# Performance work log

Measured on AMD Instinct MI355X. Metric: run time of the kernel, lower is better.

## Reference

```python
import jax, jax.numpy as jnp
import numpy as np

V, H, L, B = 32000, 512, 128, 8
PAD = 0


def setup_inputs() -> dict:
    key = jax.random.key(0)
    ks = jax.random.split(key, 20)
    s = 0.02
    inp = {
        "input_": jax.random.randint(ks[0], (B, L), 0, V),
        "encoder_inputs": jax.random.randint(ks[1], (B, L), 0, V),
        "encoder_hidden": jax.random.normal(ks[2], (1, B, H), jnp.float32),
        "encoder_outputs": jax.random.normal(ks[3], (B, L, H), jnp.float32),
        "emb_table": jax.random.normal(ks[4], (V, H), jnp.float32) * s,
        "attn_W": jax.random.normal(ks[5], (L, 2 * H), jnp.float32) * s,
        "attn_b": jnp.zeros((L,), jnp.float32),
        "comb_W": jax.random.normal(ks[6], (H, 2 * H), jnp.float32) * s,
        "comb_b": jnp.zeros((H,), jnp.float32),
        "gru_Wih": jax.random.normal(ks[7], (3 * H, H), jnp.float32) * s,
        "gru_Whh": jax.random.normal(ks[8], (3 * H, H), jnp.float32) * s,
        "gru_bih": jnp.zeros((3 * H,), jnp.float32),
        "gru_bhh": jnp.zeros((3 * H,), jnp.float32),
        "out_W": jax.random.normal(ks[9], (V, H), jnp.float32) * s,
        "out_b": jnp.zeros((V,), jnp.float32),
        "dogen_W": jax.random.normal(ks[10], (1, 3 * H), jnp.float32) * s,
        "dogen_b": jnp.zeros((1,), jnp.float32),
        "copy_W": jax.random.normal(ks[11], (1, 2 * H), jnp.float32) * s,
        "copy_b": jnp.zeros((1,), jnp.float32),
    }
    return inp


def _gru(x, h0, Wih, Whh, bih, bhh):
    # x: [B,L,H] batch_first; h0: [B,H]. PyTorch GRU gate math.
    def step(h, x_t):
        gi = x_t @ Wih.T + bih  # [B,3H]
        gh = h @ Whh.T + bhh
        i_r, i_z, i_n = jnp.split(gi, 3, axis=-1)
        h_r, h_z, h_n = jnp.split(gh, 3, axis=-1)
        r = jax.nn.sigmoid(i_r + h_r)
        z = jax.nn.sigmoid(i_z + h_z)
        n = jnp.tanh(i_n + r * h_n)
        h_new = (1.0 - z) * n + z * h
        return h_new, h_new
    _, ys = jax.lax.scan(step, h0, jnp.swapaxes(x, 0, 1))  # ys: [L,B,H]
    return jnp.swapaxes(ys, 0, 1)


def reference(input_, encoder_inputs, encoder_hidden, encoder_outputs, emb_table,
              attn_W, attn_b, comb_W, comb_b, gru_Wih, gru_Whh, gru_bih, gru_bhh,
              out_W, out_b, dogen_W, dogen_b, copy_W, copy_b):
    # Dropout is identity (eval mode).
    embedded = emb_table[input_]  # [B,L,H]
    h0 = encoder_hidden[0]  # [B,H]
    hid_exp = jnp.broadcast_to(h0[:, None, :], embedded.shape)
    attn_logits = jnp.concatenate([embedded, hid_exp], axis=2) @ attn_W.T + attn_b  # [B,L,L]
    attn_weights = jax.nn.softmax(attn_logits, axis=1)  # softmax over dim=1 (as in torch code)
    attn_applied = jnp.einsum('bij,bjh->bih', attn_weights, encoder_outputs)
    x = jnp.concatenate([embedded, attn_applied], axis=2) @ comb_W.T + comb_b
    x = jax.nn.relu(x)
    output = _gru(x, h0, gru_Wih, gru_Whh, gru_bih, gru_bhh)  # [B,L,H]
    generation_dist = jax.nn.softmax(output @ out_W.T + out_b, axis=2)  # [B,L,V]
    # get_alpha: copy_weight_proj is rank-1 over concat([e_states, d_states]);
    # compute without materializing the [B,L,L,2H] cross product.
    w_e, w_d = copy_W[0, :H], copy_W[0, H:]
    e_part = encoder_outputs @ w_e  # [B,L] (indexed by j)
    d_part = output @ w_d           # [B,L] (indexed by i)
    logits = d_part[:, :, None] + e_part[:, None, :] + copy_b[0]  # [B,L_dec,L_enc]
    pad_pen = jnp.where(encoder_inputs == PAD, -1000.0, 0.0)
    logits = logits + pad_pen[:, None, :]
    alphas = jax.nn.softmax(logits, axis=2)
    context = jnp.einsum('bij,bjh->bih', alphas, encoder_outputs)
    # scatter_add: index repeats encoder_inputs[b,i] along j, so all alpha mass
    # of row (b,i) lands at vocab id encoder_inputs[b,i].
    row_sum = alphas.sum(axis=2)  # [B,L]
    b_idx = jnp.arange(B)[:, None]
    i_idx = jnp.arange(L)[None, :]
    copy_dist = jnp.zeros((B, L, V), generation_dist.dtype).at[b_idx, i_idx, encoder_inputs].add(row_sum)
    mix = jax.nn.sigmoid(jnp.concatenate([output, context, embedded], axis=2) @ dogen_W.T + dogen_b)  # [B,L,1]
    prob = generation_dist * mix + copy_dist * (1.0 - mix)
    return prob, attn_weights
```

## Files before the change

kernel.cpp:

```cpp
#include <hip/hip_runtime.h>
#include <cstdint>

#define VDIM 32000
#define HDIM 512
#define LDIM 128
#define BDIM 8
#define MROWS 1024
#define H2 1024
#define H3 1536
#define GRU_WGS 32

typedef __bf16 bf16x8 __attribute__((ext_vector_type(8)));
typedef float f32x4 __attribute__((ext_vector_type(4)));

#define AS1 __attribute__((address_space(1)))
#define AS3 __attribute__((address_space(3)))

__device__ __forceinline__ unsigned short f2b(float x) {
  unsigned u = __builtin_bit_cast(unsigned, x);
  u += 0x7fffu + ((u >> 16) & 1u);
  return (unsigned short)(u >> 16);
}

__device__ __forceinline__ float wredS(float v) {
#pragma unroll
  for (int o = 32; o > 0; o >>= 1) v += __shfl_xor(v, o);
  return v;
}
__device__ __forceinline__ float wredM(float v) {
#pragma unroll
  for (int o = 32; o > 0; o >>= 1) v = fmaxf(v, __shfl_xor(v, o));
  return v;
}

__device__ __forceinline__ void gl_lds16(const void* g, void* l) {
  __builtin_amdgcn_global_load_lds((AS1 void*)const_cast<void*>(g), (AS3 void*)l, 16, 0, 0);
}

__global__ void cvt_kernel(const float* __restrict__ src, unsigned short* __restrict__ dst, int n4) {
  int i = blockIdx.x * 256 + threadIdx.x;
  if (i < n4) {
    float4 v = ((const float4*)src)[i];
    unsigned r0 = (unsigned)f2b(v.x) | ((unsigned)f2b(v.y) << 16);
    unsigned r1 = (unsigned)f2b(v.z) | ((unsigned)f2b(v.w) << 16);
    uint2 r; r.x = r0; r.y = r1;
    *(uint2*)(dst + (size_t)i * 4) = r;
  }
}

__global__ void init_kernel(const float* __restrict__ h0, float* __restrict__ hbuf,
                            unsigned short* __restrict__ hbufbf, float* __restrict__ rowsum,
                            int* __restrict__ cnt) {
  int tid = threadIdx.x;
  for (int i = tid; i < BDIM * HDIM; i += 256) {
    float v = h0[i];
    hbuf[i] = v;
    hbufbf[i] = f2b(v);
  }
  for (int i = tid; i < MROWS; i += 256) rowsum[i] = 0.f;
  for (int i = tid; i < 160; i += 256) cnt[i] = (i == 0) ? GRU_WGS : 0;
}

__global__ void embed_kernel(const int* __restrict__ input_, const float* __restrict__ emb,
                             float* __restrict__ emb_f, unsigned short* __restrict__ A4) {
  int m = blockIdx.x, tid = threadIdx.x;
  int tok = input_[m];
  const float* src = emb + (size_t)tok * HDIM;
  for (int k = tid; k < HDIM; k += 256) {
    float v = src[k];
    emb_f[(size_t)m * HDIM + k] = v;
    A4[(size_t)m * H2 + k] = f2b(v);
  }
}

__global__ void attn_kernel(const float* __restrict__ emb_f, const float* __restrict__ h0,
                            const float* __restrict__ attn_W, const float* __restrict__ attn_b,
                            float* __restrict__ attn_out) {
  int j = blockIdx.x, b = blockIdx.y, tid = threadIdx.x;
  int wid = tid >> 6;
  __shared__ float wj[H2];
  __shared__ float red[2];
  for (int k = tid; k < H2; k += 128) wj[k] = attn_W[(size_t)j * H2 + k];
  __syncthreads();
  float hp = 0.f;
  for (int k = tid * 4; k < tid * 4 + 4; ++k) hp += h0[b * HDIM + k] * wj[HDIM + k];
  hp = wredS(hp);
  if ((tid & 63) == 0) red[wid] = hp;
  __syncthreads();
  float hdot = red[0] + red[1];
  __syncthreads();

  int i = tid;
  const float* er = emb_f + ((size_t)(b * LDIM + i)) * HDIM;
  float acc = 0.f;
  for (int k = 0; k < HDIM; k += 4) {
    float4 e = *(const float4*)(er + k);
    acc += e.x * wj[k] + e.y * wj[k + 1] + e.z * wj[k + 2] + e.w * wj[k + 3];
  }
  float l = acc + hdot + attn_b[j];
  float mx = wredM(l);
  if ((tid & 63) == 0) red[wid] = mx;
  __syncthreads();
  mx = fmaxf(red[0], red[1]);
  __syncthreads();
  float e = __expf(l - mx);
  float s = wredS(e);
  if ((tid & 63) == 0) red[wid] = s;
  __syncthreads();
  s = red[0] + red[1];
  attn_out[(size_t)b * (LDIM * LDIM) + (size_t)i * LDIM + j] = e / s;
}

__global__ void einsum_kernel(const float* __restrict__ w, const float* __restrict__ enc,
                              float* __restrict__ outF, unsigned short* __restrict__ outBf, int mode) {
  int i = blockIdx.x, b = blockIdx.y, tid = threadIdx.x;
  __shared__ float wr[LDIM];
  if (tid < LDIM) wr[tid] = w[((size_t)(b * LDIM + i)) * LDIM + tid];
  __syncthreads();
  float a0 = 0.f, a1 = 0.f;
  const float* eb = enc + (size_t)b * LDIM * HDIM;
  for (int jj = 0; jj < LDIM; ++jj) {
    float wv = wr[jj];
    const float* er = eb + (size_t)jj * HDIM;
    a0 += wv * er[tid];
    a1 += wv * er[tid + 256];
  }
  if (mode == 0) {
    size_t base = ((size_t)(b * LDIM + i)) * H2 + HDIM;
    outBf[base + tid] = f2b(a0);
    outBf[base + tid + 256] = f2b(a1);
  } else {
    size_t base = ((size_t)(b * LDIM + i)) * HDIM;
    outF[base + tid] = a0;
    outF[base + tid + 256] = a1;
  }
}

__global__ __launch_bounds__(256) void gemm_bt(const unsigned short* __restrict__ A,
                                               const unsigned short* __restrict__ Bw, int N, int K,
                                               const float* __restrict__ bias, int mode,
                                               float* __restrict__ outF,
                                               unsigned short* __restrict__ outBf,
                                               float* __restrict__ rowsum) {
  __shared__ unsigned short sA[4096];
  __shared__ unsigned short sB[4096];
  int tid = threadIdx.x;
  int lane = tid & 63, w = tid >> 6;
  int wm = w >> 1, wn = w & 1;
  int ln15 = lane & 15, q = lane >> 4;
  int m0 = blockIdx.y * 128, n0 = blockIdx.x * 128;
  f32x4 acc[4][4] = {};
  int rowA = tid >> 2;
  int colK = (tid & 3) * 8;
  for (int kt = 0; kt < K; kt += 32) {
    __syncthreads();
    const unsigned short* ga0 = A + (size_t)(m0 + rowA) * K + kt + colK;
    const unsigned short* ga1 = A + (size_t)(m0 + 64 + rowA) * K + kt + colK;
    const unsigned short* gb0 = Bw + (size_t)(n0 + rowA) * K + kt + colK;
    const unsigned short* gb1 = Bw + (size_t)(n0 + 64 + rowA) * K + kt + colK;
    gl_lds16(ga0, sA + w * 512);
    gl_lds16(ga1, sA + 2048 + w * 512);
    gl_lds16(gb0, sB + w * 512);
    gl_lds16(gb1, sB + 2048 + w * 512);
    __syncthreads();
    bf16x8 af[4], bf[4];
#pragma unroll
    for (int t = 0; t < 4; ++t) {
      af[t] = *(const bf16x8*)(sA + (wm * 64 + t * 16 + ln15) * 32 + q * 8);
      bf[t] = *(const bf16x8*)(sB + (wn * 64 + t * 16 + ln15) * 32 + q * 8);
    }
#pragma unroll
    for (int ti = 0; ti < 4; ++ti)
#pragma unroll
      for (int tj = 0; tj < 4; ++tj)
        acc[ti][tj] = __builtin_amdgcn_mfma_f32_16x16x32_bf16(af[ti], bf[tj], acc[ti][tj], 0, 0, 0);
  }
#pragma unroll
  for (int ti = 0; ti < 4; ++ti) {
#pragma unroll
    for (int reg = 0; reg < 4; ++reg) {
      int m = m0 + wm * 64 + ti * 16 + q * 4 + reg;
      float s = 0.f;
#pragma unroll
      for (int tj = 0; tj < 4; ++tj) {
        int n = n0 + wn * 64 + tj * 16 + ln15;
        float c = acc[ti][tj][reg] + bias[n];
        if (mode == 2) {
          float e = __expf(c);
          outF[(size_t)m * N + n] = e;
          s += e;
        } else if (mode == 0) {
          outBf[(size_t)m * N + n] = f2b(fmaxf(c, 0.f));
        } else {
          outF[(size_t)m * N + n] = c;
        }
      }
      if (mode == 2) {
        s += __shfl_xor(s, 1); s += __shfl_xor(s, 2);
        s += __shfl_xor(s, 4); s += __shfl_xor(s, 8);
        if (ln15 == 0) atomicAdd(&rowsum[m], s);
      }
    }
  }
}

__global__ __launch_bounds__(64) void gru_kernel(const float* __restrict__ Whh,
                                                 const float* __restrict__ bhh,
                                                 const float* __restrict__ gi,
                                                 float* __restrict__ hbuf,
                                                 unsigned short* __restrict__ hbufbf,
                                                 float* __restrict__ outF,
                                                 unsigned short* __restrict__ Ab,
                                                 int* __restrict__ cnt) {
  __shared__ unsigned short sW[48 * 512];
  __shared__ unsigned short sH[16 * 512];
  int g = blockIdx.x, lane = threadIdx.x;
  int ln15 = lane & 15, q = lane >> 4;
  for (int idx = lane; idx < 48 * 512; idx += 64) {
    int r = idx >> 9, k = idx & 511;
    int gate = r >> 4, rl = r & 15;
    sW[idx] = f2b(Whh[(size_t)(gate * 512 + g * 16 + rl) * 512 + k]);
  }
  for (int idx = lane; idx < 8 * 512; idx += 64) sH[8 * 512 + idx] = 0;
  int j = g * 16 + ln15;
  float bh_r = bhh[j], bh_z = bhh[512 + j], bh_n = bhh[1024 + j];
  __syncthreads();

  for (int t = 0; t < 128; ++t) {
    if (lane == 0) {
      while (__hip_atomic_load(&cnt[t], __ATOMIC_ACQUIRE, __HIP_MEMORY_SCOPE_AGENT) < GRU_WGS)
        __builtin_amdgcn_s_sleep(2);
    }
    __syncthreads();
    const uint4* hb = (const uint4*)(hbufbf + (size_t)t * 4096);
    uint4* sh4 = (uint4*)sH;
#pragma unroll
    for (int i = 0; i < 8; ++i) sh4[lane + i * 64] = hb[lane + i * 64];
    __syncthreads();
    f32x4 ac0 = {}, ac1 = {}, ac2 = {};
#pragma unroll
    for (int kk = 0; kk < 512; kk += 32) {
      bf16x8 aF = *(const bf16x8*)(sH + ln15 * 512 + kk + q * 8);
      bf16x8 b0 = *(const bf16x8*)(sW + (0 + ln15) * 512 + kk + q * 8);
      bf16x8 b1 = *(const bf16x8*)(sW + ((16 + ln15) * 512) + kk + q * 8);
      bf16x8 b2 = *(const bf16x8*)(sW + ((32 + ln15) * 512) + kk + q * 8);
      ac0 = __builtin_amdgcn_mfma_f32_16x16x32_bf16(aF, b0, ac0, 0, 0, 0);
      ac1 = __builtin_amdgcn_mfma_f32_16x16x32_bf16(aF, b1, ac1, 0, 0, 0);
      ac2 = __builtin_amdgcn_mfma_f32_16x16x32_bf16(aF, b2, ac2, 0, 0, 0);
    }
    const float* hsrc = hbuf + (size_t)t * 4096;
    if (q < 2) {
#pragma unroll
      for (int reg = 0; reg < 4; ++reg) {
        int b = q * 4 + reg;
        size_t gib = ((size_t)(b * 128 + t)) * H3;
        float gir = gi[gib + j], giz = gi[gib + 512 + j], gin = gi[gib + 1024 + j];
        float rr = 1.f / (1.f + __expf(-(gir + ac0[reg] + bh_r)));
        float zz = 1.f / (1.f + __expf(-(giz + ac1[reg] + bh_z)));
        float narg = gin + rr * (ac2[reg] + bh_n);
        narg = fminf(fmaxf(narg, -20.f), 20.f);
        float te = __expf(2.f * narg);
        float nn = (te - 1.f) / (te + 1.f);
        float hp = hsrc[b * 512 + j];
        float hv = (1.f - zz) * nn + zz * hp;
        hbuf[(size_t)(t + 1) * 4096 + b * 512 + j] = hv;
        hbufbf[(size_t)(t + 1) * 4096 + b * 512 + j] = f2b(hv);
        size_t orow = ((size_t)b * 128 + t) * 512 + j;
        outF[orow] = hv;
        Ab[orow] = f2b(hv);
      }
    }
    __threadfence();
    if (lane == 0)
      __hip_atomic_fetch_add(&cnt[t + 1], 1, __ATOMIC_RELEASE, __HIP_MEMORY_SCOPE_AGENT);
  }
}

__global__ void dots_kernel(const float* __restrict__ enc, const float* __restrict__ outF,
                            const float* __restrict__ copyW, float* __restrict__ epart,
                            float* __restrict__ dpart) {
  int tid = threadIdx.x, lane = tid & 63, wid = tid >> 6;
  int gw = blockIdx.x * 4 + wid;
  for (int row = gw; row < 2048; row += 128) {
    const float* src;
    const float* wv;
    float* dst;
    int r;
    if (row < 1024) { src = enc + (size_t)row * 512; wv = copyW; dst = epart; r = row; }
    else { src = outF + (size_t)(row - 1024) * 512; wv = copyW + 512; dst = dpart; r = row - 1024; }
    float4 s1 = *(const float4*)(src + lane * 8);
    float4 s2 = *(const float4*)(src + lane * 8 + 4);
    float4 w1 = *(const float4*)(wv + lane * 8);
    float4 w2 = *(const float4*)(wv + lane * 8 + 4);
    float p = s1.x * w1.x + s1.y * w1.y + s1.z * w1.z + s1.w * w1.w +
              s2.x * w2.x + s2.y * w2.y + s2.z * w2.z + s2.w * w2.w;
    p = wredS(p);
    if (lane == 0) dst[r] = p;
  }
}

__global__ void alphas_kernel(const float* __restrict__ dpart, const float* __restrict__ epart,
                              const int* __restrict__ enc_in, const float* __restrict__ copy_b,
                              float* __restrict__ alphas) {
  int i = blockIdx.x, b = blockIdx.y, jt = threadIdx.x;
  int wid = jt >> 6;
  __shared__ float red[2];
  float l = dpart[b * 128 + i] + epart[b * 128 + jt] + copy_b[0] +
            (enc_in[b * 128 + jt] == 0 ? -1000.f : 0.f);
  float mx = wredM(l);
  if ((jt & 63) == 0) red[wid] = mx;
  __syncthreads();
  mx = fmaxf(red[0], red[1]);
  __syncthreads();
  float e = __expf(l - mx);
  float s = wredS(e);
  if ((jt & 63) == 0) red[wid] = s;
  __syncthreads();
  s = red[0] + red[1];
  alphas[((size_t)(b * 128 + i)) * 128 + jt] = e / s;
}

__global__ void mix_kernel(const float* __restrict__ outF, const float* __restrict__ ctx,
                           const float* __restrict__ emb_f, const float* __restrict__ dogenW,
                           const float* __restrict__ dogenB, float* __restrict__ mixb) {
  int tid = threadIdx.x, lane = tid & 63, wid = tid >> 6;
  int gw = blockIdx.x * 4 + wid;
  for (int row = gw; row < 1024; row += 64) {
    int k = lane * 8;
    const float* o = outF + (size_t)row * 512;
    const float* c = ctx + (size_t)row * 512;
    const float* e = emb_f + (size_t)row * 512;
    float p = 0.f;
#pragma unroll
    for (int u = 0; u < 8; ++u)
      p += o[k + u] * dogenW[k + u] + c[k + u] * dogenW[512 + k + u] + e[k + u] * dogenW[1024 + k + u];
    p = wredS(p);
    if (lane == 0) mixb[row] = 1.f / (1.f + __expf(-(p + dogenB[0])));
  }
}

__global__ void final_kernel(float* __restrict__ prob, const float* __restrict__ mixb,
                             const float* __restrict__ rowsum, const int* __restrict__ enc_in) {
  int row = blockIdx.y;
  int v = blockIdx.x * 256 + threadIdx.x;
  float mx = mixb[row], rs = rowsum[row];
  size_t idx = (size_t)row * VDIM + v;
  float val = prob[idx] * (mx / rs);
  if (v == enc_in[row]) val += 1.f - mx;
  prob[idx] = val;
}

extern "C" void kernel_launch(void* const* d_in, const int* in_sizes, int n_in, void* d_out,
                              int out_size, void* d_ws, size_t ws_size, hipStream_t stream) {
  const int* input_ = (const int*)d_in[0];
  const int* enc_in = (const int*)d_in[1];
  const float* enc_h = (const float*)d_in[2];
  const float* enc_out = (const float*)d_in[3];
  const float* emb = (const float*)d_in[4];
  const float* attn_W = (const float*)d_in[5];
  const float* attn_b = (const float*)d_in[6];
  const float* comb_W = (const float*)d_in[7];
  const float* comb_b = (const float*)d_in[8];
  const float* Wih = (const float*)d_in[9];
  const float* Whh = (const float*)d_in[10];
  const float* bih = (const float*)d_in[11];
  const float* bhh = (const float*)d_in[12];
  const float* out_W = (const float*)d_in[13];
  const float* out_b = (const float*)d_in[14];
  const float* dogen_W = (const float*)d_in[15];
  const float* dogen_b = (const float*)d_in[16];
  const float* copy_W = (const float*)d_in[17];
  const float* copy_b = (const float*)d_in[18];

  float* prob = (float*)d_out;
  float* attn_out = prob + (size_t)MROWS * VDIM;

  char* ws = (char*)d_ws;
  size_t off = 0;
  auto alloc = [&](size_t bytes) {
    off = (off + 255) & ~(size_t)255;
    void* p = ws + off;
    off += bytes;
    return p;
  };
  unsigned short* outW_bf = (unsigned short*)alloc((size_t)VDIM * HDIM * 2);
  unsigned short* combW_bf = (unsigned short*)alloc((size_t)HDIM * H2 * 2);
  unsigned short* Wih_bf = (unsigned short*)alloc((size_t)H3 * HDIM * 2);
  unsigned short* A4 = (unsigned short*)alloc((size_t)MROWS * H2 * 2);
  unsigned short* xbf = (unsigned short*)alloc((size_t)MROWS * HDIM * 2);
  unsigned short* Ab = (unsigned short*)alloc((size_t)MROWS * HDIM * 2);
  float* emb_f = (float*)alloc((size_t)MROWS * HDIM * 4);
  float* gi = (float*)alloc((size_t)MROWS * H3 * 4);
  float* outF = (float*)alloc((size_t)MROWS * HDIM * 4);
  float* hbuf = (float*)alloc((size_t)129 * 4096 * 4);
  unsigned short* hbufbf = (unsigned short*)alloc((size_t)129 * 4096 * 2);
  int* cnt = (int*)alloc(1024);
  float* rowsum = (float*)alloc(4096);
  float* epart = (float*)alloc(4096);
  float* dpart = (float*)alloc(4096);
  float* alphas = (float*)alloc((size_t)MROWS * LDIM * 4);
  float* ctx = (float*)alloc((size_t)MROWS * HDIM * 4);
  float* mixb = (float*)alloc(4096);

  cvt_kernel<<<(VDIM * HDIM / 4 + 255) / 256, 256, 0, stream>>>(out_W, outW_bf, VDIM * HDIM / 4);
  cvt_kernel<<<(HDIM * H2 / 4 + 255) / 256, 256, 0, stream>>>(comb_W, combW_bf, HDIM * H2 / 4);
  cvt_kernel<<<(H3 * HDIM / 4 + 255) / 256, 256, 0, stream>>>(Wih, Wih_bf, H3 * HDIM / 4);
  init_kernel<<<1, 256, 0, stream>>>(enc_h, hbuf, hbufbf, rowsum, cnt);
  embed_kernel<<<MROWS, 256, 0, stream>>>(input_, emb, emb_f, A4);
  attn_kernel<<<dim3(LDIM, BDIM), 128, 0, stream>>>(emb_f, enc_h, attn_W, attn_b, attn_out);
  einsum_kernel<<<dim3(LDIM, BDIM), 256, 0, stream>>>(attn_out, enc_out, nullptr, A4, 0);
  gemm_bt<<<dim3(4, 8), 256, 0, stream>>>(A4, combW_bf, HDIM, H2, comb_b, 0, nullptr, xbf, nullptr);
  gemm_bt<<<dim3(12, 8), 256, 0, stream>>>(xbf, Wih_bf, H3, HDIM, bih, 1, gi, nullptr, nullptr);
  gru_kernel<<<GRU_WGS, 64, 0, stream>>>(Whh, bhh, gi, hbuf, hbufbf, outF, Ab, cnt);
  gemm_bt<<<dim3(VDIM / 128, 8), 256, 0, stream>>>(Ab, outW_bf, VDIM, HDIM, out_b, 2, prob, nullptr, rowsum);
  dots_kernel<<<32, 256, 0, stream>>>(enc_out, outF, copy_W, epart, dpart);
  alphas_kernel<<<dim3(LDIM, BDIM), 128, 0, stream>>>(dpart, epart, enc_in, copy_b, alphas);
  einsum_kernel<<<dim3(LDIM, BDIM), 256, 0, stream>>>(alphas, enc_out, ctx, nullptr, 1);
  mix_kernel<<<16, 256, 0, stream>>>(outF, ctx, emb_f, dogen_W, dogen_b, mixb);
  final_kernel<<<dim3(VDIM / 256, MROWS), 256, 0, stream>>>(prob, mixb, rowsum, enc_in);
}
```

Before: 1.319 ms.

## Streamline GRU recurrence: register h state, direct global A loads, prefetch gi

The GRU kernel now keeps the fp32 hidden state in registers and drops the fp32 hbuf history. It also loads the bf16 h fragments for the MFMA straight from global memory into registers, removing the LDS staging and its extra barrier. The gi gate inputs are prefetched before the spin-wait, the weight layout in LDS is rearranged so each lane reads contiguously, and the threadfence is dropped with output stores moved after the release. The h buffer is padded to 16 rows per step and zeroed by a new kernel. Dropping the threadfence leans on the release atomic to order the bf16 h stores, which is a subtle correctness risk.

After: 1.347 ms. +2.1%, slower.

```diff
diff --git a/kernel.cpp b/kernel.cpp
--- a/kernel.cpp
+++ b/kernel.cpp
@@ -9,6 +9,7 @@
 #define H2 1024
 #define H3 1536
 #define GRU_WGS 32
+#define HSTEP 8192
 
 typedef __bf16 bf16x8 __attribute__((ext_vector_type(8)));
 typedef float f32x4 __attribute__((ext_vector_type(4)));
@@ -48,14 +49,19 @@
   }
 }
 
-__global__ void init_kernel(const float* __restrict__ h0, float* __restrict__ hbuf,
-                            unsigned short* __restrict__ hbufbf, float* __restrict__ rowsum,
-                            int* __restrict__ cnt) {
+__global__ void hzero_kernel(unsigned short* __restrict__ hbufbf) {
+  size_t i = (size_t)blockIdx.x * 256 + threadIdx.x;
+  uint4 z = {0, 0, 0, 0};
+  size_t n8 = (size_t)129 * HSTEP / 8;
+  if (i < n8) ((uint4*)hbufbf)[i] = z;
+}
+
+__global__ void init_kernel(const float* __restrict__ h0, unsigned short* __restrict__ hbufbf,
+                            float* __restrict__ rowsum, int* __restrict__ cnt) {
   int tid = threadIdx.x;
   for (int i = tid; i < BDIM * HDIM; i += 256) {
-    float v = h0[i];
-    hbuf[i] = v;
-    hbufbf[i] = f2b(v);
+    int b = i >> 9, k = i & 511;
+    hbufbf[b * 512 + k] = f2b(h0[i]);
   }
   for (int i = tid; i < MROWS; i += 256) rowsum[i] = 0.f;
   for (int i = tid; i < 160; i += 256) cnt[i] = (i == 0) ? GRU_WGS : 0;
@@ -207,72 +213,91 @@
 __global__ __launch_bounds__(64) void gru_kernel(const float* __restrict__ Whh,
                                                  const float* __restrict__ bhh,
                                                  const float* __restrict__ gi,
-                                                 float* __restrict__ hbuf,
+                                                 const float* __restrict__ h0,
                                                  unsigned short* __restrict__ hbufbf,
                                                  float* __restrict__ outF,
                                                  unsigned short* __restrict__ Ab,
                                                  int* __restrict__ cnt) {
-  __shared__ unsigned short sW[48 * 512];
-  __shared__ unsigned short sH[16 * 512];
+  __shared__ unsigned short sW[3 * 16 * 64 * 8];
   int g = blockIdx.x, lane = threadIdx.x;
   int ln15 = lane & 15, q = lane >> 4;
-  for (int idx = lane; idx < 48 * 512; idx += 64) {
-    int r = idx >> 9, k = idx & 511;
-    int gate = r >> 4, rl = r & 15;
-    sW[idx] = f2b(Whh[(size_t)(gate * 512 + g * 16 + rl) * 512 + k]);
-  }
-  for (int idx = lane; idx < 8 * 512; idx += 64) sH[8 * 512 + idx] = 0;
   int j = g * 16 + ln15;
+#pragma unroll 1
+  for (int gate = 0; gate < 3; ++gate) {
+#pragma unroll 1
+    for (int kk = 0; kk < 16; ++kk) {
+      const float* src = Whh + (size_t)(gate * 512 + g * 16 + ln15) * 512 + kk * 32 + q * 8;
+      float4 v0 = *(const float4*)src, v1 = *(const float4*)(src + 4);
+      unsigned short* dst = sW + (size_t)((gate * 16 + kk) * 64 + lane) * 8;
+      dst[0] = f2b(v0.x); dst[1] = f2b(v0.y); dst[2] = f2b(v0.z); dst[3] = f2b(v0.w);
+      dst[4] = f2b(v1.x); dst[5] = f2b(v1.y); dst[6] = f2b(v1.z); dst[7] = f2b(v1.w);
+    }
+  }
   float bh_r = bhh[j], bh_z = bhh[512 + j], bh_n = bhh[1024 + j];
+  float hreg[4];
+  if (q < 2) {
+#pragma unroll
+    for (int reg = 0; reg < 4; ++reg) hreg[reg] = h0[(q * 4 + reg) * 512 + j];
+  }
   __syncthreads();
 
   for (int t = 0; t < 128; ++t) {
+    float gir[4], giz[4], gin[4];
+    if (q < 2) {
+#pragma unroll
+      for (int reg = 0; reg < 4; ++reg) {
+        size_t gib = ((size_t)((q * 4 + reg) * 128 + t)) * H3;
+        gir[reg] = gi[gib + j];
+        giz[reg] = gi[gib + 512 + j];
+        gin[reg] = gi[gib + 1024 + j];
+      }
+    }
     if (lane == 0) {
       while (__hip_atomic_load(&cnt[t], __ATOMIC_ACQUIRE, __HIP_MEMORY_SCOPE_AGENT) < GRU_WGS)
-        __builtin_amdgcn_s_sleep(2);
+        __builtin_amdgcn_s_sleep(1);
     }
     __syncthreads();
-    const uint4* hb = (const uint4*)(hbufbf + (size_t)t * 4096);
-    uint4* sh4 = (uint4*)sH;
-#pragma unroll
-    for (int i = 0; i < 8; ++i) sh4[lane + i * 64] = hb[lane + i * 64];
-    __syncthreads();
+    const unsigned short* hT = hbufbf + (size_t)t * HSTEP + ln15 * 512 + q * 8;
+    bf16x8 aF[16];
+#pragma unroll
+    for (int kk = 0; kk < 16; ++kk) aF[kk] = *(const bf16x8*)(hT + kk * 32);
     f32x4 ac0 = {}, ac1 = {}, ac2 = {};
 #pragma unroll
-    for (int kk = 0; kk < 512; kk += 32) {
-      bf16x8 aF = *(const bf16x8*)(sH + ln15 * 512 + kk + q * 8);
-      bf16x8 b0 = *(const bf16x8*)(sW + (0 + ln15) * 512 + kk + q * 8);
-      bf16x8 b1 = *(const bf16x8*)(sW + ((16 + ln15) * 512) + kk + q * 8);
-      bf16x8 b2 = *(const bf16x8*)(sW + ((32 + ln15) * 512) + kk + q * 8);
-      ac0 = __builtin_amdgcn_mfma_f32_16x16x32_bf16(aF, b0, ac0, 0, 0, 0);
-      ac1 = __builtin_amdgcn_mfma_f32_16x16x32_bf16(aF, b1, ac1, 0, 0, 0);
-      ac2 = __builtin_amdgcn_mfma_f32_16x16x32_bf16(aF, b2, ac2, 0, 0, 0);
-    }
-    const float* hsrc = hbuf + (size_t)t * 4096;
+    for (int kk = 0; kk < 16; ++kk) {
+      bf16x8 b0 = *(const bf16x8*)(sW + (size_t)((0 * 16 + kk) * 64 + lane) * 8);
+      bf16x8 b1 = *(const bf16x8*)(sW + (size_t)((1 * 16 + kk) * 64 + lane) * 8);
+      bf16x8 b2 = *(const bf16x8*)(sW + (size_t)((2 * 16 + kk) * 64 + lane) * 8);
+      ac0 = __builtin_amdgcn_mfma_f32_16x16x32_bf16(aF[kk], b0, ac0, 0, 0, 0);
+      ac1 = __builtin_amdgcn_mfma_f32_16x16x32_bf16(aF[kk], b1, ac1, 0, 0, 0);
+      ac2 = __builtin_amdgcn_mfma_f32_16x16x32_bf16(aF[kk], b2, ac2, 0, 0, 0);
+    }
+    float hv[4];
     if (q < 2) {
 #pragma unroll
       for (int reg = 0; reg < 4; ++reg) {
         int b = q * 4 + reg;
-        size_t gib = ((size_t)(b * 128 + t)) * H3;
-        float gir = gi[gib + j], giz = gi[gib + 512 + j], gin = gi[gib + 1024 + j];
-        float rr = 1.f / (1.f + __expf(-(gir + ac0[reg] + bh_r)));
-        float zz = 1.f / (1.f + __expf(-(giz + ac1[reg] + bh_z)));
-        float narg = gin + rr * (ac2[reg] + bh_n);
+        float rr = 1.f / (1.f + __expf(-(gir[reg] + ac0[reg] + bh_r)));
+        float zz = 1.f / (1.f + __expf(-(giz[reg] + ac1[reg] + bh_z)));
+        float narg = gin[reg] + rr * (ac2[reg] + bh_n);
         narg = fminf(fmaxf(narg, -20.f), 20.f);
         float te = __expf(2.f * narg);
         float nn = (te - 1.f) / (te + 1.f);
-        float hp = hsrc[b * 512 + j];
-        float hv = (1.f - zz) * nn + zz * hp;
-        hbuf[(size_t)(t + 1) * 4096 + b * 512 + j] = hv;
-        hbufbf[(size_t)(t + 1) * 4096 + b * 512 + j] = f2b(hv);
-        size_t orow = ((size_t)b * 128 + t) * 512 + j;
-        outF[orow] = hv;
-        Ab[orow] = f2b(hv);
+        hv[reg] = (1.f - zz) * nn + zz * hreg[reg];
+        hreg[reg] = hv[reg];
+        hbufbf[(size_t)(t + 1) * HSTEP + b * 512 + j] = f2b(hv[reg]);
       }
     }
-    __threadfence();
     if (lane == 0)
       __hip_atomic_fetch_add(&cnt[t + 1], 1, __ATOMIC_RELEASE, __HIP_MEMORY_SCOPE_AGENT);
+    if (q < 2) {
+#pragma unroll
+      for (int reg = 0; reg < 4; ++reg) {
+        int b = q * 4 + reg;
+        size_t orow = ((size_t)b * 128 + t) * 512 + j;
+        outF[orow] = hv[reg];
+        Ab[orow] = f2b(hv[reg]);
+      }
+    }
   }
 }
 
@@ -392,8 +417,7 @@
   float* emb_f = (float*)alloc((size_t)MROWS * HDIM * 4);
   float* gi = (float*)alloc((size_t)MROWS * H3 * 4);
   float* outF = (float*)alloc((size_t)MROWS * HDIM * 4);
-  float* hbuf = (float*)alloc((size_t)129 * 4096 * 4);
-  unsigned short* hbufbf = (unsigned short*)alloc((size_t)129 * 4096 * 2);
+  unsigned short* hbufbf = (unsigned short*)alloc((size_t)129 * HSTEP * 2);
   int* cnt = (int*)alloc(1024);
   float* rowsum = (float*)alloc(4096);
   float* epart = (float*)alloc(4096);
@@ -405,13 +429,17 @@
   cvt_kernel<<<(VDIM * HDIM / 4 + 255) / 256, 256, 0, stream>>>(out_W, outW_bf, VDIM * HDIM / 4);
   cvt_kernel<<<(HDIM * H2 / 4 + 255) / 256, 256, 0, stream>>>(comb_W, combW_bf, HDIM * H2 / 4);
   cvt_kernel<<<(H3 * HDIM / 4 + 255) / 256, 256, 0, stream>>>(Wih, Wih_bf, H3 * HDIM / 4);
-  init_kernel<<<1, 256, 0, stream>>>(enc_h, hbuf, hbufbf, rowsum, cnt);
+  {
+    int n8 = (int)((size_t)129 * HSTEP / 8);
+    hzero_kernel<<<(n8 + 255) / 256, 256, 0, stream>>>(hbufbf);
+  }
+  init_kernel<<<1, 256, 0, stream>>>(enc_h, hbufbf, rowsum, cnt);
   embed_kernel<<<MROWS, 256, 0, stream>>>(input_, emb, emb_f, A4);
   attn_kernel<<<dim3(LDIM, BDIM), 128, 0, stream>>>(emb_f, enc_h, attn_W, attn_b, attn_out);
   einsum_kernel<<<dim3(LDIM, BDIM), 256, 0, stream>>>(attn_out, enc_out, nullptr, A4, 0);
   gemm_bt<<<dim3(4, 8), 256, 0, stream>>>(A4, combW_bf, HDIM, H2, comb_b, 0, nullptr, xbf, nullptr);
   gemm_bt<<<dim3(12, 8), 256, 0, stream>>>(xbf, Wih_bf, H3, HDIM, bih, 1, gi, nullptr, nullptr);
-  gru_kernel<<<GRU_WGS, 64, 0, stream>>>(Whh, bhh, gi, hbuf, hbufbf, outF, Ab, cnt);
+  gru_kernel<<<GRU_WGS, 64, 0, stream>>>(Whh, bhh, gi, enc_h, hbufbf, outF, Ab, cnt);
   gemm_bt<<<dim3(VDIM / 128, 8), 256, 0, stream>>>(Ab, outW_bf, VDIM, HDIM, out_b, 2, prob, nullptr, rowsum);
   dots_kernel<<<32, 256, 0, stream>>>(enc_out, outF, copy_W, epart, dpart);
   alphas_kernel<<<dim3(LDIM, BDIM), 128, 0, stream>>>(dpart, epart, enc_in, copy_b, alphas);
```
